# Performance work log

Hardware: AMD Instinct MI355X
Metric: run time of the kernel (lower is better)

## Reference

```python
import jax, jax.numpy as jnp
import numpy as np

B, H, W, C = 8, 128, 128, 256
NH = 8
HD = C // NH
WS = 8           # window size
SS = 4           # shift size
N = WS * WS      # tokens per window
SCALE = HD ** -0.5
EPS = 1e-5


def _rel_pos_index():
    coords = np.stack(np.meshgrid(np.arange(WS), np.arange(WS), indexing='ij'))  # [2,WS,WS]
    cf = coords.reshape(2, -1)                                                   # [2,N]
    rel = (cf[:, :, None] - cf[:, None, :]).transpose(1, 2, 0)                   # [N,N,2]
    rel[..., 0] += WS - 1
    rel[..., 1] += WS - 1
    rel[..., 0] *= 2 * WS - 1
    return rel.sum(-1)  # [N,N] indices into (2*WS-1)^2 table

RPI = jnp.asarray(_rel_pos_index())


def _attn_mask():
    img = np.zeros((H, W))
    slices = (slice(0, -WS), slice(-WS, -SS), slice(-SS, None))
    cnt = 0
    for hs in slices:
        for ws_ in slices:
            img[hs, ws_] = cnt
            cnt += 1
    mw = img.reshape(H // WS, WS, W // WS, WS).transpose(0, 2, 1, 3).reshape(-1, N)  # [nW,N]
    am = mw[:, None, :] - mw[:, :, None]
    return jnp.asarray(np.where(am != 0, -100.0, 0.0).astype(np.float32))  # [nW,N,N]

ATTN_MASK = _attn_mask()


def _ln(x, g, b):
    m = jnp.mean(x, -1, keepdims=True)
    v = jnp.var(x, -1, keepdims=True)
    return (x - m) * jax.lax.rsqrt(v + EPS) * g + b


def setup_inputs() -> dict:
    key = jax.random.key(0)
    ks = jax.random.split(key, 8)
    s = 0.02
    return {
        'x': jax.random.normal(ks[0], (B, H * W, C), jnp.float32),
        'qkv_w': jax.random.normal(ks[1], (C, 3 * C), jnp.float32) * s,
        'qkv_b': jnp.zeros((3 * C,), jnp.float32),
        'proj_w': jax.random.normal(ks[2], (C, C), jnp.float32) * s,
        'proj_b': jnp.zeros((C,), jnp.float32),
        'rpb': jax.random.normal(ks[3], ((2 * WS - 1) ** 2, NH), jnp.float32) * s,
        'g1': jnp.ones((C,), jnp.float32), 'b1': jnp.zeros((C,), jnp.float32),
        'g2': jnp.ones((C,), jnp.float32), 'b2': jnp.zeros((C,), jnp.float32),
        'fc1_w': jax.random.normal(ks[4], (C, 4 * C), jnp.float32) * s,
        'fc1_b': jnp.zeros((4 * C,), jnp.float32),
        'fc2_w': jax.random.normal(ks[5], (4 * C, C), jnp.float32) * s,
        'fc2_b': jnp.zeros((C,), jnp.float32),
    }


def reference(x, qkv_w, qkv_b, proj_w, proj_b, rpb, g1, b1, g2, b2,
              fc1_w, fc1_b, fc2_w, fc2_b):
    nW = (H // WS) * (W // WS)
    shortcut = x
    h = _ln(x, g1, b1).reshape(B, H, W, C)
    # cyclic shift
    h = jnp.roll(h, (-SS, -SS), axis=(1, 2))
    # window partition -> (B*nW, N, C)
    win = h.reshape(B, H // WS, WS, W // WS, WS, C).transpose(0, 1, 3, 2, 4, 5).reshape(-1, N, C)
    qkv = (win @ qkv_w + qkv_b).reshape(-1, N, 3, NH, HD).transpose(2, 0, 3, 1, 4)  # [3,B_,NH,N,HD]
    q, k, v = qkv[0] * SCALE, qkv[1], qkv[2]
    attn = jnp.einsum('bhnd,bhmd->bhnm', q, k)                    # [B_,NH,N,N]
    bias = rpb[RPI].transpose(2, 0, 1)                             # [NH,N,N]
    attn = attn + bias[None]
    attn = attn.reshape(B, nW, NH, N, N) + ATTN_MASK[None, :, None]
    attn = jax.nn.softmax(attn.reshape(-1, NH, N, N), axis=-1)
    out = jnp.einsum('bhnm,bhmd->bhnd', attn, v).transpose(0, 2, 1, 3).reshape(-1, N, C)
    out = out @ proj_w + proj_b
    # window reverse + reverse shift
    out = out.reshape(B, H // WS, W // WS, WS, WS, C).transpose(0, 1, 3, 2, 4, 5).reshape(B, H, W, C)
    out = jnp.roll(out, (SS, SS), axis=(1, 2)).reshape(B, H * W, C)
    x = shortcut + out
    hm = _ln(x, g2, b2)
    hm = jax.nn.gelu(hm @ fc1_w + fc1_b, approximate=False) @ fc2_w + fc2_b
    return x + hm
```

## Files before the change

kernel.cpp:

```cpp
#include <hip/hip_runtime.h>
#include <math.h>


#define NWIN_TOTAL 2048
#define TOK_TOTAL  131072
#define SCALE_Q    0.17677669529663687f
#define LOG2E      1.4426950408889634f

typedef unsigned short u16;
typedef __attribute__((ext_vector_type(4))) unsigned short u16x4;
typedef __attribute__((ext_vector_type(8))) unsigned short u16x8;
typedef __attribute__((ext_vector_type(8))) short bf16x8;
typedef __attribute__((ext_vector_type(4))) float f32x4;

#define AS1 __attribute__((address_space(1)))
#define AS3 __attribute__((address_space(3)))
#define GLOAD_LDS16(g, l) \
  __builtin_amdgcn_global_load_lds((const AS1 unsigned int*)(g), (AS3 unsigned int*)(l), 16, 0, 0)

__device__ __forceinline__ float bf2f(u16 u) {
  union { unsigned int i; float f; } c; c.i = ((unsigned int)u) << 16; return c.f;
}
__device__ __forceinline__ u16 f2bf(float f) {
  union { float f; unsigned int i; } c; c.f = f;
  return (u16)((c.i + 0x7fff + ((c.i >> 16) & 1)) >> 16);
}
__device__ __forceinline__ int regid3(int h) { return h < 120 ? 0 : (h < 124 ? 1 : 2); }
__device__ __forceinline__ float gelu_f(float v) {
  return 0.5f * v * (1.0f + erff(v * 0.7071067811865475f));
}

__device__ __forceinline__ int win_tok_to_t(int g, int n) {
  int b = g >> 8, wi = g & 255;
  int wr = wi >> 4, wc = wi & 15;
  int hs = wr * 8 + (n >> 3), ws2 = wc * 8 + (n & 7);
  int h = (hs + 4) & 127, w = (ws2 + 4) & 127;
  return (b << 14) + (h << 7) + w;
}

__global__ __launch_bounds__(256)
void wconv_kernel(const float* __restrict__ w, u16* __restrict__ wt, int K, int N)
{
  int i = blockIdx.x * 256 + threadIdx.x;
  if (i >= K * N) return;
  int k = i / N, n = i - k * N;
  wt[(size_t)n * K + k] = f2bf(w[i]);
}

__global__ __launch_bounds__(256)
void ln1_kernel(const float* __restrict__ x, const float* __restrict__ g1,
                const float* __restrict__ b1, u16* __restrict__ outw, int g0)
{
  int gid  = blockIdx.x * 4 + (threadIdx.x >> 6);
  int lane = threadIdx.x & 63;
  int g = g0 + (gid >> 6);
  int t = win_tok_to_t(g, gid & 63);
  float4 v = ((const float4*)x)[(size_t)t * 64 + lane];
  float s = v.x + v.y + v.z + v.w;
  float q = v.x * v.x + v.y * v.y + v.z * v.z + v.w * v.w;
#pragma unroll
  for (int m = 1; m < 64; m <<= 1) { s += __shfl_xor(s, m, 64); q += __shfl_xor(q, m, 64); }
  float mean = s * 0.00390625f;
  float var  = q * 0.00390625f - mean * mean;
  float rstd = rsqrtf(var + 1e-5f);
  float4 gg = ((const float4*)g1)[lane];
  float4 bb = ((const float4*)b1)[lane];
  u16x4 o;
  o.x = f2bf((v.x - mean) * rstd * gg.x + bb.x);
  o.y = f2bf((v.y - mean) * rstd * gg.y + bb.y);
  o.z = f2bf((v.z - mean) * rstd * gg.z + bb.z);
  o.w = f2bf((v.w - mean) * rstd * gg.w + bb.w);
  *(u16x4*)(outw + (size_t)gid * 256 + lane * 4) = o;
}

struct BArgs {
  const u16* A; const u16* Bt; const float* bias;
  u16* q; u16* k; u16* v;
  int M, N, K;
};

__global__ __launch_bounds__(256)
void qkv_gemm(BArgs a)
{
  __shared__ u16 As[2][4096];
  __shared__ u16 Bs[2][4096];
  const int tid  = threadIdx.x;
  const int wid  = tid >> 6, lane = tid & 63;
  const int wr   = wid >> 1, wc = wid & 1;
  const int gx = gridDim.x;
  const int nwg = gx * gridDim.y;
  const int p = blockIdx.y * gx + blockIdx.x;
  const int qq = nwg >> 3, rr = nwg & 7, xcd = p & 7;
  const int l = (xcd < rr ? xcd * (qq + 1) : rr * (qq + 1) + (xcd - rr) * qq) + (p >> 3);
  const int rowBase = (l / gx) * 128;
  const int colBase = (l % gx) * 128;
  const int lr = lane >> 2;
  const int lc = (lane & 3) * 8;
  const int l15 = lane & 15, lhi = lane >> 4;

  f32x4 acc[4][4];
#pragma unroll
  for (int m = 0; m < 4; ++m)
#pragma unroll
    for (int n = 0; n < 4; ++n) acc[m][n] = (f32x4){0.f, 0.f, 0.f, 0.f};

  const int nkt = a.K >> 5;

#define STAGE(buf, kk)                                                          \
  {                                                                             \
    _Pragma("unroll")                                                           \
    for (int i = 0; i < 2; ++i) {                                               \
      const int srow = wid * 32 + i * 16;                                       \
      GLOAD_LDS16(a.A  + (size_t)(rowBase + srow + lr) * a.K + (kk) + lc,       \
                  &As[buf][srow * 32]);                                         \
      GLOAD_LDS16(a.Bt + (size_t)(colBase + srow + lr) * a.K + (kk) + lc,       \
                  &Bs[buf][srow * 32]);                                         \
    }                                                                           \
  }

  STAGE(0, 0);
  __syncthreads();
  int cur = 0;
  for (int kt = 0; kt < nkt; ++kt) {
    if (kt + 1 < nkt) STAGE(cur ^ 1, (kt + 1) << 5);
    bf16x8 af[4], bfr[4];
#pragma unroll
    for (int m = 0; m < 4; ++m)
      af[m] = *(const bf16x8*)&As[cur][(wr * 64 + m * 16 + l15) * 32 + lhi * 8];
#pragma unroll
    for (int n = 0; n < 4; ++n)
      bfr[n] = *(const bf16x8*)&Bs[cur][(wc * 64 + n * 16 + l15) * 32 + lhi * 8];
#pragma unroll
    for (int m = 0; m < 4; ++m)
#pragma unroll
      for (int n = 0; n < 4; ++n)
        acc[m][n] = __builtin_amdgcn_mfma_f32_16x16x32_bf16(af[m], bfr[n], acc[m][n], 0, 0, 0);
    __syncthreads();
    cur ^= 1;
  }
#undef STAGE

#pragma unroll
  for (int n = 0; n < 4; ++n) {
    const int col16 = colBase + wc * 64 + n * 16;
    const float bv = a.bias[col16 + l15];
    u16* qdst = nullptr; float scl = 1.f; size_t obase = 0;
    int vsel = 0;
    {
      const int s = col16 >> 8, head = (col16 >> 5) & 7, hd = col16 & 31;
      if (s == 2) {
        vsel = 1;
        obase = ((size_t)head << 11) + (size_t)(hd + l15) * 64;
      } else {
        qdst = (s == 0) ? a.q : a.k;
        if (s == 0) scl = SCALE_Q * LOG2E;
        obase = ((size_t)head << 11) + hd + l15;
      }
    }
#pragma unroll
    for (int m = 0; m < 4; ++m) {
      const int row0 = rowBase + wr * 64 + m * 16 + lhi * 4;
      if (vsel) {
        const int gw = row0 >> 6, tok0 = row0 & 63;
        u16x4 pk;
#pragma unroll
        for (int r = 0; r < 4; ++r) pk[r] = f2bf(acc[m][n][r] + bv);
        *(u16x4*)&a.v[((size_t)gw << 14) + obase + tok0] = pk;
        continue;
      }
#pragma unroll
      for (int r = 0; r < 4; ++r) {
        const int row = row0 + r;
        const int gw = row >> 6, tok = row & 63;
        qdst[((size_t)gw << 14) + obase + ((size_t)tok << 5)] = f2bf((acc[m][n][r] + bv) * scl);
      }
    }
  }
}

__global__ __launch_bounds__(512)
void awp_kernel(const u16* __restrict__ qb, const u16* __restrict__ kb,
                const u16* __restrict__ vt, const float* __restrict__ rpb,
                const u16* __restrict__ pjT, const float* __restrict__ pjb,
                const float* __restrict__ x, float* __restrict__ out, int g0)
{
  __shared__ union {
    u16 pl[8][2048];
    u16 aoL[16384];
    float rep[8192];
  } sb;
  __shared__ float rl[1800];
  const int tid = threadIdx.x, hh = tid >> 6, lane = tid & 63;
  const int l15 = lane & 15, g = lane >> 4;
  const int bw = blockIdx.x;

  for (int i = tid; i < 1800; i += 512) {
    unsigned int h2 = (unsigned)i / 225u;
    unsigned int rem = (unsigned)i - h2 * 225u;
    unsigned int aa = rem / 15u, bb = rem - aa * 15u;
    rl[i] = rpb[(aa * 15u + 14u - bb) * 8u + h2] * LOG2E;
  }
  __syncthreads();

  const size_t base = ((size_t)(bw * 8 + hh)) << 11;

  bf16x8 qf[4], kf[4];
#pragma unroll
  for (int f = 0; f < 4; ++f) {
    qf[f] = *(const bf16x8*)(qb + base + (size_t)(f * 16 + l15) * 32 + g * 8);
    kf[f] = *(const bf16x8*)(kb + base + (size_t)(f * 16 + l15) * 32 + g * 8);
  }
  f32x4 acc[4][4];
#pragma unroll
  for (int mf = 0; mf < 4; ++mf)
#pragma unroll
    for (int nf = 0; nf < 4; ++nf) acc[mf][nf] = (f32x4){0.f, 0.f, 0.f, 0.f};
#pragma unroll
  for (int mf = 0; mf < 4; ++mf)
#pragma unroll
    for (int nf = 0; nf < 4; ++nf)
      acc[mf][nf] = __builtin_amdgcn_mfma_f32_16x16x32_bf16(kf[mf], qf[nf], acc[mf][nf], 0, 0, 0);

  const int gwin = g0 + bw;
  const int wrw = (gwin >> 4) & 15, wcw = gwin & 15;
  const bool edge = (wrw == 15) || (wcw == 15);
  const int i2b = g >> 1;
  const int j2b = (g & 1) * 4;
#pragma unroll
  for (int nf = 0; nf < 4; ++nf) {
    const int n = nf * 16 + l15;
    const int i1 = n >> 3, j1 = n & 7;
    const int rid1 = edge ? regid3(wrw * 8 + i1) * 3 + regid3(wcw * 8 + j1) : 0;
#pragma unroll
    for (int mf = 0; mf < 4; ++mf) {
      const int i2 = mf * 2 + i2b;
      const int ib = hh * 225 + (i1 - i2 + 7) * 15 + (j2b - j1 + 7);
      const int r2a = edge ? regid3(wrw * 8 + i2) * 3 : 0;
#pragma unroll
      for (int r = 0; r < 4; ++r) {
        float b = rl[ib + r];
        if (edge) {
          int rid2 = r2a + regid3(wcw * 8 + j2b + r);
          if (rid2 != rid1) b -= 144.2695f;
        }
        acc[mf][nf][r] += b;
      }
    }
  }

  float inv[4];
#pragma unroll
  for (int nf = 0; nf < 4; ++nf) {
    float m0 = -1e30f;
#pragma unroll
    for (int mf = 0; mf < 4; ++mf)
#pragma unroll
      for (int r = 0; r < 4; ++r) m0 = fmaxf(m0, acc[mf][nf][r]);
    m0 = fmaxf(m0, __shfl_xor(m0, 16, 64));
    m0 = fmaxf(m0, __shfl_xor(m0, 32, 64));
    float s = 0.f;
#pragma unroll
    for (int mf = 0; mf < 4; ++mf)
#pragma unroll
      for (int r = 0; r < 4; ++r) {
        float p = exp2f(acc[mf][nf][r] - m0);
        acc[mf][nf][r] = p;
        s += p;
      }
    s += __shfl_xor(s, 16, 64);
    s += __shfl_xor(s, 32, 64);
    inv[nf] = 1.f / s;
  }

  bf16x8 vf[2][2];
#pragma unroll
  for (int df = 0; df < 2; ++df)
#pragma unroll
    for (int ks = 0; ks < 2; ++ks)
      vf[df][ks] = *(const bf16x8*)(vt + base + (size_t)(df * 16 + l15) * 64 + ks * 32 + g * 8);
  f32x4 accO[4][2];
#pragma unroll
  for (int nf = 0; nf < 4; ++nf)
#pragma unroll
    for (int df = 0; df < 2; ++df) accO[nf][df] = (f32x4){0.f, 0.f, 0.f, 0.f};
  char* plw = (char*)sb.pl[hh];
#pragma unroll
  for (int ks = 0; ks < 2; ++ks) {
#pragma unroll
    for (int nf = 0; nf < 4; ++nf) {
      const int n = nf * 16 + l15;
      const int swz = (n & 3) << 4;
#pragma unroll
      for (int mm = 0; mm < 2; ++mm) {
        const int mf = ks * 2 + mm;
        float p0 = acc[mf][nf][0] * inv[nf], p1 = acc[mf][nf][1] * inv[nf];
        float p2 = acc[mf][nf][2] * inv[nf], p3 = acc[mf][nf][3] * inv[nf];
        unsigned int pa, pb;
        asm("v_cvt_pk_bf16_f32 %0, %1, %2" : "=v"(pa) : "v"(p0), "v"(p1));
        asm("v_cvt_pk_bf16_f32 %0, %1, %2" : "=v"(pb) : "v"(p2), "v"(p3));
        uint2 w; w.x = pa; w.y = pb;
        *(uint2*)(plw + ((n * 64 + mm * 32 + g * 8) ^ swz)) = w;
      }
    }
#pragma unroll
    for (int nf = 0; nf < 4; ++nf) {
      const int n = nf * 16 + l15;
      const int swz = (n & 3) << 4;
      bf16x8 pf = *(const bf16x8*)(plw + ((n * 64 + g * 16) ^ swz));
#pragma unroll
      for (int df = 0; df < 2; ++df)
        accO[nf][df] = __builtin_amdgcn_mfma_f32_16x16x32_bf16(pf, vf[df][ks], accO[nf][df], 0, 0, 0);
    }
  }

  __syncthreads();
#pragma unroll
  for (int nf = 0; nf < 4; ++nf)
#pragma unroll
    for (int r = 0; r < 4; ++r) {
      const int tok = nf * 16 + g * 4 + r;
#pragma unroll
      for (int df = 0; df < 2; ++df) {
        const int ch = hh * 32 + df * 16 + l15;
        *(u16*)((char*)sb.aoL + tok * 512 + ((((ch >> 3) ^ (tok & 7))) << 4) + (ch & 7) * 2) =
            f2bf(accO[nf][df][r]);
      }
    }
  __syncthreads();

  f32x4 pacc[4][2];
#pragma unroll
  for (int mf = 0; mf < 4; ++mf)
#pragma unroll
    for (int of = 0; of < 2; ++of) pacc[mf][of] = (f32x4){0.f, 0.f, 0.f, 0.f};
  const u16* pB = pjT + (size_t)(hh * 32) * 256;
#pragma unroll
  for (int ks = 0; ks < 8; ++ks) {
    bf16x8 af[4], bwf[2];
#pragma unroll
    for (int mf = 0; mf < 4; ++mf) {
      const int tok = mf * 16 + l15;
      af[mf] = *(const bf16x8*)((char*)sb.aoL + tok * 512 + (((ks * 4 + g) ^ (tok & 7)) << 4));
    }
#pragma unroll
    for (int of = 0; of < 2; ++of)
      bwf[of] = *(const bf16x8*)(pB + (size_t)(of * 16 + l15) * 256 + ks * 32 + g * 8);
#pragma unroll
    for (int mf = 0; mf < 4; ++mf)
#pragma unroll
      for (int of = 0; of < 2; ++of)
        pacc[mf][of] = __builtin_amdgcn_mfma_f32_16x16x32_bf16(af[mf], bwf[of], pacc[mf][of], 0, 0, 0);
  }

#pragma unroll
  for (int hp = 0; hp < 2; ++hp) {
    __syncthreads();
#pragma unroll
    for (int mm = 0; mm < 2; ++mm) {
      const int mf = hp * 2 + mm;
#pragma unroll
      for (int of = 0; of < 2; ++of) {
        const int oc = hh * 32 + of * 16 + l15;
        const float bv = pjb[oc];
#pragma unroll
        for (int r = 0; r < 4; ++r) {
          const int row = mm * 16 + g * 4 + r;
          *(float*)((char*)sb.rep + ((row * 1024 + oc * 4) ^ ((row & 3) << 4))) =
              pacc[mf][of][r] + bv;
        }
      }
    }
    __syncthreads();
    const int rowl = tid >> 4, coll = (tid & 15) * 16;
    const int tok = hp * 32 + rowl;
    const int t = win_tok_to_t(g0 + bw, tok);
    const float* xs = x + (size_t)t * 256 + coll;
    float* od = out + (size_t)t * 256 + coll;
#pragma unroll
    for (int i = 0; i < 4; ++i) {
      float4 rv = *(const float4*)((char*)sb.rep +
                    ((rowl * 1024 + (coll + i * 4) * 4) ^ ((rowl & 3) << 4)));
      float4 xv = ((const float4*)xs)[i];
      ((float4*)od)[i] = make_float4(rv.x + xv.x, rv.y + xv.y, rv.z + xv.z, rv.w + xv.w);
    }
  }
}

__global__ __launch_bounds__(256)
void mlp_kernel(float* io, const u16* __restrict__ w1t, const u16* __restrict__ w2t,
                const float* __restrict__ fb1, const float* __restrict__ fb2,
                const float* __restrict__ g2, const float* __restrict__ bt2)
{
  __shared__ u16 Aln[16384];
  __shared__ u16 Hs[8192];
  const int tid = threadIdx.x, wid = tid >> 6, lane = tid & 63;
  const int l15 = lane & 15, g = lane >> 4;
  const int t0 = blockIdx.x * 64;

  {
    const int row = tid >> 2;
    const int cq = (tid & 3) * 64;
    const float* src = io + (size_t)(t0 + row) * 256 + cq;
    float vals[64];
    float s = 0.f, q = 0.f;
#pragma unroll
    for (int i = 0; i < 16; ++i) {
      float4 v = ((const float4*)src)[i];
      vals[i*4] = v.x; vals[i*4+1] = v.y; vals[i*4+2] = v.z; vals[i*4+3] = v.w;
      s += v.x + v.y + v.z + v.w;
      q += v.x*v.x + v.y*v.y + v.z*v.z + v.w*v.w;
    }
    s += __shfl_xor(s, 1, 64); q += __shfl_xor(q, 1, 64);
    s += __shfl_xor(s, 2, 64); q += __shfl_xor(q, 2, 64);
    float mean = s * 0.00390625f;
    float rstd = rsqrtf(q * 0.00390625f - mean * mean + 1e-5f);
#pragma unroll
    for (int i = 0; i < 8; ++i) {
      const int col = cq + i * 8;
      u16x8 o;
#pragma unroll
      for (int j = 0; j < 8; ++j)
        o[j] = f2bf((vals[i*8+j] - mean) * rstd * g2[col+j] + bt2[col+j]);
      const int gran = col >> 3;
      *(u16x8*)((char*)Aln + row * 512 + ((gran ^ (row & 7)) << 4)) = o;
    }
  }
  __syncthreads();

  f32x4 acc2[4][4];
#pragma unroll
  for (int m = 0; m < 4; ++m)
#pragma unroll
    for (int n = 0; n < 4; ++n) acc2[m][n] = (f32x4){0.f, 0.f, 0.f, 0.f};

  for (int c = 0; c < 8; ++c) {
    f32x4 acc1[2][4];
#pragma unroll
    for (int hf = 0; hf < 2; ++hf)
#pragma unroll
      for (int tf = 0; tf < 4; ++tf) acc1[hf][tf] = (f32x4){0.f, 0.f, 0.f, 0.f};
    const u16* w1base = w1t + (size_t)(c * 128 + wid * 32) * 256;
#pragma unroll
    for (int ks = 0; ks < 8; ++ks) {
      bf16x8 af[2], bfr[4];
#pragma unroll
      for (int hf = 0; hf < 2; ++hf)
        af[hf] = *(const bf16x8*)(w1base + (size_t)(hf * 16 + l15) * 256 + ks * 32 + g * 8);
#pragma unroll
      for (int tf = 0; tf < 4; ++tf) {
        const int tok = tf * 16 + l15;
        const int gran = ks * 4 + g;
        bfr[tf] = *(const bf16x8*)&Aln[tok * 256 + ((gran ^ (tok & 7)) << 3)];
      }
#pragma unroll
      for (int hf = 0; hf < 2; ++hf)
#pragma unroll
        for (int tf = 0; tf < 4; ++tf)
          acc1[hf][tf] = __builtin_amdgcn_mfma_f32_16x16x32_bf16(af[hf], bfr[tf], acc1[hf][tf], 0, 0, 0);
    }
    __syncthreads();
#pragma unroll
    for (int hf = 0; hf < 2; ++hf) {
      const int hcl = wid * 32 + hf * 16 + g * 4;
      const float b0 = fb1[c * 128 + hcl];
      const float b1 = fb1[c * 128 + hcl + 1];
      const float b2v = fb1[c * 128 + hcl + 2];
      const float b3 = fb1[c * 128 + hcl + 3];
#pragma unroll
      for (int tf = 0; tf < 4; ++tf) {
        const int tok = tf * 16 + l15;
        float p0 = gelu_f(acc1[hf][tf][0] + b0);
        float p1 = gelu_f(acc1[hf][tf][1] + b1);
        float p2 = gelu_f(acc1[hf][tf][2] + b2v);
        float p3 = gelu_f(acc1[hf][tf][3] + b3);
        unsigned int pa, pb;
        asm("v_cvt_pk_bf16_f32 %0, %1, %2" : "=v"(pa) : "v"(p0), "v"(p1));
        asm("v_cvt_pk_bf16_f32 %0, %1, %2" : "=v"(pb) : "v"(p2), "v"(p3));
        uint2 w; w.x = pa; w.y = pb;
        *(uint2*)((char*)Hs + tok * 256 + (((hcl >> 3) ^ (tok & 7)) << 4) + ((hcl & 4) << 1)) = w;
      }
    }
    __syncthreads();
    const u16* w2base = w2t + (size_t)(wid * 64) * 1024 + c * 128;
#pragma unroll
    for (int hk = 0; hk < 4; ++hk) {
      bf16x8 ah[4], bw[4];
#pragma unroll
      for (int tf = 0; tf < 4; ++tf) {
        const int tok = tf * 16 + l15;
        const int gran = hk * 4 + g;
        ah[tf] = *(const bf16x8*)&Hs[tok * 128 + ((gran ^ (tok & 7)) << 3)];
      }
#pragma unroll
      for (int of = 0; of < 4; ++of)
        bw[of] = *(const bf16x8*)(w2base + (size_t)(of * 16 + l15) * 1024 + hk * 32 + g * 8);
#pragma unroll
      for (int tf = 0; tf < 4; ++tf)
#pragma unroll
        for (int of = 0; of < 4; ++of)
          acc2[tf][of] = __builtin_amdgcn_mfma_f32_16x16x32_bf16(ah[tf], bw[of], acc2[tf][of], 0, 0, 0);
    }
  }

#pragma unroll
  for (int tf = 0; tf < 4; ++tf) {
#pragma unroll
    for (int of = 0; of < 4; ++of) {
      const int oc = wid * 64 + of * 16 + l15;
      const float bv = fb2[oc];
#pragma unroll
      for (int r = 0; r < 4; ++r) {
        const size_t off = (size_t)(t0 + tf * 16 + g * 4 + r) * 256 + oc;
        io[off] = acc2[tf][of][r] + bv + io[off];
      }
    }
  }
}

extern "C" void kernel_launch(void* const* d_in, const int* in_sizes, int n_in,
                              void* d_out, int out_size, void* d_ws, size_t ws_size,
                              hipStream_t stream)
{
  const float* x      = (const float*)d_in[0];
  const float* qkv_w  = (const float*)d_in[1];
  const float* qkv_b  = (const float*)d_in[2];
  const float* proj_w = (const float*)d_in[3];
  const float* proj_b = (const float*)d_in[4];
  const float* rpb    = (const float*)d_in[5];
  const float* g1     = (const float*)d_in[6];
  const float* b1     = (const float*)d_in[7];
  const float* g2     = (const float*)d_in[8];
  const float* b2     = (const float*)d_in[9];
  const float* fc1_w  = (const float*)d_in[10];
  const float* fc1_b  = (const float*)d_in[11];
  const float* fc2_w  = (const float*)d_in[12];
  const float* fc2_b  = (const float*)d_in[13];
  float* out = (float*)d_out;
  char* ws = (char*)d_ws;

  u16* qkvT  = (u16*)ws;
  u16* projT = qkvT + 196608;
  u16* fc1T  = projT + 65536;
  u16* fc2T  = fc1T + 262144;
  char* pb = (char*)(fc2T + 262144);
  size_t used = 1572864ULL;
  size_t R = ws_size > used ? ws_size - used : 0;

  wconv_kernel<<<(196608 + 255) / 256, 256, 0, stream>>>(qkv_w, qkvT, 256, 768);
  wconv_kernel<<<(65536  + 255) / 256, 256, 0, stream>>>(proj_w, projT, 256, 256);
  wconv_kernel<<<(262144 + 255) / 256, 256, 0, stream>>>(fc1_w, fc1T, 256, 1024);
  wconv_kernel<<<(262144 + 255) / 256, 256, 0, stream>>>(fc2_w, fc2T, 1024, 256);

  int Gc = 2048;
  while (Gc > 2 && (size_t)Gc * 131072ULL > R) Gc >>= 1;

  u16* ln1w = (u16*)pb;
  u16* qb = ln1w + (size_t)Gc * 16384;
  u16* kb = qb + (size_t)Gc * 16384;
  u16* vb = kb + (size_t)Gc * 16384;

  for (int g0 = 0; g0 < NWIN_TOTAL; g0 += Gc) {
    int nT = Gc * 64;
    ln1_kernel<<<nT / 4, 256, 0, stream>>>(x, g1, b1, ln1w, g0);

    BArgs qa = {}; qa.A = ln1w; qa.Bt = qkvT; qa.bias = qkv_b;
    qa.q = qb; qa.k = kb; qa.v = vb; qa.M = nT; qa.N = 768; qa.K = 256;
    qkv_gemm<<<dim3(6, nT / 128), 256, 0, stream>>>(qa);

    awp_kernel<<<Gc, 512, 0, stream>>>(qb, kb, vb, rpb, projT, proj_b, x, out, g0);
  }

  mlp_kernel<<<TOK_TOTAL / 64, 256, 0, stream>>>(out, fc1T, fc2T, fc1_b, fc2_b, g2, b2);
}
```

Baseline: 705.6 us.

## Double-buffer MLP hidden tile and swap erf GELU for sigmoid approximation

```diff
diff --git a/kernel.cpp b/kernel.cpp
--- a/kernel.cpp
+++ b/kernel.cpp
@@ -27,7 +27,8 @@
 }
 __device__ __forceinline__ int regid3(int h) { return h < 120 ? 0 : (h < 124 ? 1 : 2); }
 __device__ __forceinline__ float gelu_f(float v) {
-  return 0.5f * v * (1.0f + erff(v * 0.7071067811865475f));
+  float t = exp2f(v * fmaf(v * v, 0.10294423f, 2.3022082f));
+  return v * t * __builtin_amdgcn_rcpf(t + 1.0f);
 }
 
 __device__ __forceinline__ int win_tok_to_t(int g, int n) {
@@ -392,7 +393,7 @@
                 const float* __restrict__ g2, const float* __restrict__ bt2)
 {
   __shared__ u16 Aln[16384];
-  __shared__ u16 Hs[8192];
+  __shared__ u16 Hs[2][8192];
   const int tid = threadIdx.x, wid = tid >> 6, lane = tid & 63;
   const int l15 = lane & 15, g = lane >> 4;
   const int t0 = blockIdx.x * 64;
@@ -425,82 +426,106 @@
       *(u16x8*)((char*)Aln + row * 512 + ((gran ^ (row & 7)) << 4)) = o;
     }
   }
+
+  f32x4 acc2[4][4];
+#pragma unroll
+  for (int m = 0; m < 4; ++m)
+#pragma unroll
+    for (int n = 0; n < 4; ++n) acc2[m][n] = (f32x4){0.f, 0.f, 0.f, 0.f};
+  f32x4 acc1[2][4];
+
+#define MGEMM1(c)                                                                \
+  {                                                                              \
+    _Pragma("unroll")                                                            \
+    for (int hf = 0; hf < 2; ++hf)                                               \
+      _Pragma("unroll")                                                          \
+      for (int tf = 0; tf < 4; ++tf) acc1[hf][tf] = (f32x4){0.f, 0.f, 0.f, 0.f}; \
+    const u16* w1base = w1t + (size_t)((c) * 128 + wid * 32) * 256;              \
+    _Pragma("unroll")                                                            \
+    for (int ks = 0; ks < 8; ++ks) {                                             \
+      bf16x8 af[2], bfr[4];                                                      \
+      _Pragma("unroll")                                                          \
+      for (int hf = 0; hf < 2; ++hf)                                             \
+        af[hf] = *(const bf16x8*)(w1base + (size_t)(hf * 16 + l15) * 256 + ks * 32 + g * 8); \
+      _Pragma("unroll")                                                          \
+      for (int tf = 0; tf < 4; ++tf) {                                           \
+        const int tok = tf * 16 + l15;                                           \
+        const int gran = ks * 4 + g;                                             \
+        bfr[tf] = *(const bf16x8*)&Aln[tok * 256 + ((gran ^ (tok & 7)) << 3)];   \
+      }                                                                          \
+      _Pragma("unroll")                                                          \
+      for (int hf = 0; hf < 2; ++hf)                                             \
+        _Pragma("unroll")                                                        \
+        for (int tf = 0; tf < 4; ++tf)                                           \
+          acc1[hf][tf] = __builtin_amdgcn_mfma_f32_16x16x32_bf16(af[hf], bfr[tf], acc1[hf][tf], 0, 0, 0); \
+    }                                                                            \
+  }
+
+#define MPACK(c)                                                                 \
+  {                                                                              \
+    char* hdst = (char*)Hs[(c) & 1];                                             \
+    _Pragma("unroll")                                                            \
+    for (int hf = 0; hf < 2; ++hf) {                                             \
+      const int hcl = wid * 32 + hf * 16 + g * 4;                                \
+      const float b0 = fb1[(c) * 128 + hcl];                                     \
+      const float b1 = fb1[(c) * 128 + hcl + 1];                                 \
+      const float b2v = fb1[(c) * 128 + hcl + 2];                                \
+      const float b3 = fb1[(c) * 128 + hcl + 3];                                 \
+      _Pragma("unroll")                                                          \
+      for (int tf = 0; tf < 4; ++tf) {                                           \
+        const int tok = tf * 16 + l15;                                           \
+        float p0 = gelu_f(acc1[hf][tf][0] + b0);                                 \
+        float p1 = gelu_f(acc1[hf][tf][1] + b1);                                 \
+        float p2 = gelu_f(acc1[hf][tf][2] + b2v);                                \
+        float p3 = gelu_f(acc1[hf][tf][3] + b3);                                 \
+        unsigned int pa, pb;                                                     \
+        asm("v_cvt_pk_bf16_f32 %0, %1, %2" : "=v"(pa) : "v"(p0), "v"(p1));       \
+        asm("v_cvt_pk_bf16_f32 %0, %1, %2" : "=v"(pb) : "v"(p2), "v"(p3));       \
+        uint2 w; w.x = pa; w.y = pb;                                             \
+        *(uint2*)(hdst + tok * 256 + (((hcl >> 3) ^ (tok & 7)) << 4) + ((hcl & 4) << 1)) = w; \
+      }                                                                          \
+    }                                                                            \
+  }
+
+#define MGEMM2(c)                                                                \
+  {                                                                              \
+    const char* hsrc = (const char*)Hs[(c) & 1];                                 \
+    const u16* w2base = w2t + (size_t)(wid * 64) * 1024 + (c) * 128;             \
+    _Pragma("unroll")                                                            \
+    for (int hk = 0; hk < 4; ++hk) {                                             \
+      bf16x8 ah[4], bw[4];                                                       \
+      _Pragma("unroll")                                                          \
+      for (int tf = 0; tf < 4; ++tf) {                                           \
+        const int tok = tf * 16 + l15;                                           \
+        const int gran = hk * 4 + g;                                             \
+        ah[tf] = *(const bf16x8*)(hsrc + tok * 256 + ((gran ^ (tok & 7)) << 4)); \
+      }                                                                          \
+      _Pragma("unroll")                                                          \
+      for (int of = 0; of < 4; ++of)                                             \
+        bw[of] = *(const bf16x8*)(w2base + (size_t)(of * 16 + l15) * 1024 + hk * 32 + g * 8); \
+      _Pragma("unroll")                                                          \
+      for (int tf = 0; tf < 4; ++tf)                                             \
+        _Pragma("unroll")                                                        \
+        for (int of = 0; of < 4; ++of)                                           \
+          acc2[tf][of] = __builtin_amdgcn_mfma_f32_16x16x32_bf16(ah[tf], bw[of], acc2[tf][of], 0, 0, 0); \
+    }                                                                            \
+  }
+
   __syncthreads();
-
-  f32x4 acc2[4][4];
-#pragma unroll
-  for (int m = 0; m < 4; ++m)
-#pragma unroll
-    for (int n = 0; n < 4; ++n) acc2[m][n] = (f32x4){0.f, 0.f, 0.f, 0.f};
-
-  for (int c = 0; c < 8; ++c) {
-    f32x4 acc1[2][4];
-#pragma unroll
-    for (int hf = 0; hf < 2; ++hf)
-#pragma unroll
-      for (int tf = 0; tf < 4; ++tf) acc1[hf][tf] = (f32x4){0.f, 0.f, 0.f, 0.f};
-    const u16* w1base = w1t + (size_t)(c * 128 + wid * 32) * 256;
-#pragma unroll
-    for (int ks = 0; ks < 8; ++ks) {
-      bf16x8 af[2], bfr[4];
-#pragma unroll
-      for (int hf = 0; hf < 2; ++hf)
-        af[hf] = *(const bf16x8*)(w1base + (size_t)(hf * 16 + l15) * 256 + ks * 32 + g * 8);
-#pragma unroll
-      for (int tf = 0; tf < 4; ++tf) {
-        const int tok = tf * 16 + l15;
-        const int gran = ks * 4 + g;
-        bfr[tf] = *(const bf16x8*)&Aln[tok * 256 + ((gran ^ (tok & 7)) << 3)];
-      }
-#pragma unroll
-      for (int hf = 0; hf < 2; ++hf)
-#pragma unroll
-        for (int tf = 0; tf < 4; ++tf)
-          acc1[hf][tf] = __builtin_amdgcn_mfma_f32_16x16x32_bf16(af[hf], bfr[tf], acc1[hf][tf], 0, 0, 0);
-    }
+  MGEMM1(0);
+  MPACK(0);
+  __syncthreads();
+#pragma unroll
+  for (int c = 1; c < 8; ++c) {
+    MGEMM2(c - 1);
+    MGEMM1(c);
+    MPACK(c);
     __syncthreads();
-#pragma unroll
-    for (int hf = 0; hf < 2; ++hf) {
-      const int hcl = wid * 32 + hf * 16 + g * 4;
-      const float b0 = fb1[c * 128 + hcl];
-      const float b1 = fb1[c * 128 + hcl + 1];
-      const float b2v = fb1[c * 128 + hcl + 2];
-      const float b3 = fb1[c * 128 + hcl + 3];
-#pragma unroll
-      for (int tf = 0; tf < 4; ++tf) {
-        const int tok = tf * 16 + l15;
-        float p0 = gelu_f(acc1[hf][tf][0] + b0);
-        float p1 = gelu_f(acc1[hf][tf][1] + b1);
-        float p2 = gelu_f(acc1[hf][tf][2] + b2v);
-        float p3 = gelu_f(acc1[hf][tf][3] + b3);
-        unsigned int pa, pb;
-        asm("v_cvt_pk_bf16_f32 %0, %1, %2" : "=v"(pa) : "v"(p0), "v"(p1));
-        asm("v_cvt_pk_bf16_f32 %0, %1, %2" : "=v"(pb) : "v"(p2), "v"(p3));
-        uint2 w; w.x = pa; w.y = pb;
-        *(uint2*)((char*)Hs + tok * 256 + (((hcl >> 3) ^ (tok & 7)) << 4) + ((hcl & 4) << 1)) = w;
-      }
-    }
-    __syncthreads();
-    const u16* w2base = w2t + (size_t)(wid * 64) * 1024 + c * 128;
-#pragma unroll
-    for (int hk = 0; hk < 4; ++hk) {
-      bf16x8 ah[4], bw[4];
-#pragma unroll
-      for (int tf = 0; tf < 4; ++tf) {
-        const int tok = tf * 16 + l15;
-        const int gran = hk * 4 + g;
-        ah[tf] = *(const bf16x8*)&Hs[tok * 128 + ((gran ^ (tok & 7)) << 3)];
-      }
-#pragma unroll
-      for (int of = 0; of < 4; ++of)
-        bw[of] = *(const bf16x8*)(w2base + (size_t)(of * 16 + l15) * 1024 + hk * 32 + g * 8);
-#pragma unroll
-      for (int tf = 0; tf < 4; ++tf)
-#pragma unroll
-        for (int of = 0; of < 4; ++of)
-          acc2[tf][of] = __builtin_amdgcn_mfma_f32_16x16x32_bf16(ah[tf], bw[of], acc2[tf][of], 0, 0, 0);
-    }
-  }
+  }
+  MGEMM2(7);
+#undef MGEMM1
+#undef MPACK
+#undef MGEMM2
 
 #pragma unroll
   for (int tf = 0; tf < 4; ++tf) {
```

After: 787.3 us. +11.6%, slower.
